# Kernel tuning notes

Hardware: AMD Instinct MI355X
Metric: run time of the kernel (lower is better)

Reference implementation:

```python
import jax, jax.numpy as jnp
import numpy as np

NUM_CENTROID = 64
HIDDEN = 768
MAX_SEQ = 128
D = MAX_SEQ * HIDDEN  # 98304 flattened feature dim
NUM_ITERS = 10        # fixed Lloyd iterations (original loops to tol; fixed for jit)


def _cdist(x, c):
    x2 = jnp.sum(x * x, axis=-1, keepdims=True)          # [N,1]
    c2 = jnp.sum(c * c, axis=-1)                          # [K]
    d2 = x2 + c2[None, :] - 2.0 * (x @ c.T)               # [N,K]
    return jnp.sqrt(jnp.maximum(d2, 0.0))


def setup_inputs() -> dict:
    key = jax.random.key(0)
    k1, k2 = jax.random.split(key)
    x = jax.random.normal(k1, (1024, MAX_SEQ, HIDDEN), dtype=jnp.float32)
    # centroid table initialized as Normal(mean=0.07, std=0.39) per the module
    centroid = 0.07 + 0.39 * jax.random.normal(k2, (NUM_CENTROID, D), dtype=jnp.float32)
    return {"x": x, "centroid": centroid}


def reference(x, centroid):
    X = x.reshape(-1, D)                                  # [N, D]
    N = X.shape[0]
    # 'resuming' branch: snap each centroid to its nearest sample
    dis0 = _cdist(X, centroid)                            # [N, K]
    choice_points = jnp.argmin(dis0, axis=0)              # [K]
    state = X[choice_points]                              # [K, D]
    ones = jnp.ones((N,), dtype=X.dtype)

    def step(state, _):
        dis = _cdist(X, state)                            # [N, K]
        choice = jnp.argmin(dis, axis=1)                  # [N]
        sums = jax.ops.segment_sum(X, choice, num_segments=NUM_CENTROID)   # [K, D]
        counts = jax.ops.segment_sum(ones, choice, num_segments=NUM_CENTROID)  # [K]
        nonempty = counts[:, None] > 0
        new_state = jnp.where(nonempty, sums / jnp.maximum(counts[:, None], 1.0), state)
        return new_state, choice

    state, choices = jax.lax.scan(step, state, None, length=NUM_ITERS)
    # returns (new centroids, final cluster assignments) like the module
    return state, choices[-1]
```

## Files before the change

kernel.cpp:

```cpp
#include <hip/hip_runtime.h>
#include <cstddef>
#include <cstdint>


#define N_PTS  1024
#define K_C    64
#define D_DIM  98304
#define ITERS  10
#define SPLITD 64
#define BM     64
#define DC     64
#define LDSP   72
#define NCHK   96
#define CCHK   12
#define NGRP   32
#define SHPG   6
#define SHW    512
#define NCHT   96
#define NPAIR  36
#define GT     128
#define GDC    32

typedef __attribute__((ext_vector_type(8))) short bf16x8;
typedef __attribute__((ext_vector_type(8))) unsigned short ushort8;
typedef __attribute__((ext_vector_type(4))) float f32x4;

__device__ __forceinline__ unsigned short f2bf(float x) {
    unsigned u = __float_as_uint(x);
    u = (u + 0x7FFFu + ((u >> 16) & 1u)) >> 16;
    return (unsigned short)u;
}
__device__ __forceinline__ float bf2f(unsigned short b) {
    return __uint_as_float((unsigned)b << 16);
}
__device__ __forceinline__ void cvt2(float x, unsigned short& h, unsigned short& l) {
    h = f2bf(x);
    l = f2bf(x - bf2f(h));
}

__device__ __forceinline__ void gload_lds16(const unsigned short* g, char* l) {
    __builtin_amdgcn_global_load_lds(
        (const __attribute__((address_space(1))) unsigned int*)g,
        (__attribute__((address_space(3))) unsigned int*)l, 16, 0, 0);
}

__device__ __forceinline__ float block_sum256(float s) {
    #pragma unroll
    for (int o = 32; o; o >>= 1) s += __shfl_down(s, o);
    __shared__ float red[4];
    int lane = threadIdx.x & 63, w = threadIdx.x >> 6;
    if (lane == 0) red[w] = s;
    __syncthreads();
    return red[0] + red[1] + red[2] + red[3];
}

__global__ __launch_bounds__(256) void convert_kernel(const float* __restrict__ A,
                                                      unsigned short* __restrict__ Ph,
                                                      unsigned short* __restrict__ Pl,
                                                      float* __restrict__ sq_part) {
    const int n = blockIdx.x, j = blockIdx.y;
    const size_t base = (size_t)n * D_DIM + (size_t)j * 8192;
    const int t = threadIdx.x;
    float ss = 0.f;
    #pragma unroll
    for (int i = 0; i < 4; ++i) {
        size_t e = base + (size_t)i * 2048 + t * 8;
        float4 a = *reinterpret_cast<const float4*>(A + e);
        float4 b = *reinterpret_cast<const float4*>(A + e + 4);
        ss += a.x*a.x + a.y*a.y + a.z*a.z + a.w*a.w;
        ss += b.x*b.x + b.y*b.y + b.z*b.z + b.w*b.w;
        ushort4 h0, l0, h1, l1;
        cvt2(a.x, h0.x, l0.x); cvt2(a.y, h0.y, l0.y);
        cvt2(a.z, h0.z, l0.z); cvt2(a.w, h0.w, l0.w);
        cvt2(b.x, h1.x, l1.x); cvt2(b.y, h1.y, l1.y);
        cvt2(b.z, h1.z, l1.z); cvt2(b.w, h1.w, l1.w);
        *reinterpret_cast<ushort4*>(Ph + e)     = h0;
        *reinterpret_cast<ushort4*>(Ph + e + 4) = h1;
        *reinterpret_cast<ushort4*>(Pl + e)     = l0;
        *reinterpret_cast<ushort4*>(Pl + e + 4) = l1;
    }
    ss = block_sum256(ss);
    if (t == 0) sq_part[n * CCHK + j] = ss;
}

__global__ __launch_bounds__(256) void reduce_sq_kernel(const float* __restrict__ sq_part,
                                                        float* __restrict__ out, int rows) {
    int n = blockIdx.x * 256 + threadIdx.x;
    if (n >= rows) return;
    float s = 0.f;
    #pragma unroll
    for (int j = 0; j < CCHK; ++j) s += sq_part[n * CCHK + j];
    out[n] = s;
}

__global__ __launch_bounds__(256) void mfma_dot_kernel(const unsigned short* __restrict__ Xh,
                                                       const unsigned short* __restrict__ Xl,
                                                       const unsigned short* __restrict__ Sh,
                                                       const unsigned short* __restrict__ Sl,
                                                       float* __restrict__ partial) {
    __shared__ alignas(16) short Bh[K_C][LDSP];
    __shared__ alignas(16) short Bl[K_C][LDSP];

    const int seg = blockIdx.x, nblk = blockIdx.y;
    const int t = threadIdx.x;
    const int wid = t >> 6, lane = t & 63;
    const int d_begin = seg * (D_DIM / SPLITD);
    const int NCH = (D_DIM / SPLITD) / DC;

    const int arow = nblk * BM + wid * 16 + (lane & 15);
    const int ko = (lane >> 4) * 8;
    const unsigned short* xh = Xh + (size_t)arow * D_DIM;
    const unsigned short* xl = Xl + (size_t)arow * D_DIM;

    const int sr = t >> 2, sc = (t & 3) * 16;
    const unsigned short* shp = Sh + (size_t)sr * D_DIM;
    const unsigned short* slp = Sl + (size_t)sr * D_DIM;

    ushort8 s0, s1, s2, s3;
    bf16x8 aEh0, aEh1, aEl0, aEl1;
    bf16x8 aOh0, aOh1, aOl0, aOl1;

    auto loadB = [&](int d0) {
        s0 = *reinterpret_cast<const ushort8*>(shp + d0 + sc);
        s1 = *reinterpret_cast<const ushort8*>(shp + d0 + sc + 8);
        s2 = *reinterpret_cast<const ushort8*>(slp + d0 + sc);
        s3 = *reinterpret_cast<const ushort8*>(slp + d0 + sc + 8);
    };
    auto storeB = [&]() {
        *reinterpret_cast<ushort8*>(&Bh[sr][sc])     = s0;
        *reinterpret_cast<ushort8*>(&Bh[sr][sc + 8]) = s1;
        *reinterpret_cast<ushort8*>(&Bl[sr][sc])     = s2;
        *reinterpret_cast<ushort8*>(&Bl[sr][sc + 8]) = s3;
    };

    f32x4 acc[4];
    #pragma unroll
    for (int i = 0; i < 4; ++i) acc[i] = f32x4{0.f, 0.f, 0.f, 0.f};

    #define LOADA(bh0, bh1, bl0, bl1, d0)                                        \
        bh0 = *reinterpret_cast<const bf16x8*>(xh + (d0) + ko);                  \
        bh1 = *reinterpret_cast<const bf16x8*>(xh + (d0) + 32 + ko);             \
        bl0 = *reinterpret_cast<const bf16x8*>(xl + (d0) + ko);                  \
        bl1 = *reinterpret_cast<const bf16x8*>(xl + (d0) + 32 + ko);

    #define MFMAS(ah0, ah1, al0, al1)                                            \
        _Pragma("unroll")                                                        \
        for (int nb = 0; nb < 4; ++nb) {                                         \
            const int br = nb * 16 + (lane & 15);                                \
            bf16x8 bh = *reinterpret_cast<const bf16x8*>(&Bh[br][ko]);           \
            bf16x8 bl = *reinterpret_cast<const bf16x8*>(&Bl[br][ko]);           \
            acc[nb] = __builtin_amdgcn_mfma_f32_16x16x32_bf16(ah0, bh, acc[nb], 0, 0, 0); \
            acc[nb] = __builtin_amdgcn_mfma_f32_16x16x32_bf16(ah0, bl, acc[nb], 0, 0, 0); \
            acc[nb] = __builtin_amdgcn_mfma_f32_16x16x32_bf16(al0, bh, acc[nb], 0, 0, 0); \
        }                                                                        \
        _Pragma("unroll")                                                        \
        for (int nb = 0; nb < 4; ++nb) {                                         \
            const int br = nb * 16 + (lane & 15);                                \
            bf16x8 bh = *reinterpret_cast<const bf16x8*>(&Bh[br][32 + ko]);      \
            bf16x8 bl = *reinterpret_cast<const bf16x8*>(&Bl[br][32 + ko]);      \
            acc[nb] = __builtin_amdgcn_mfma_f32_16x16x32_bf16(ah1, bh, acc[nb], 0, 0, 0); \
            acc[nb] = __builtin_amdgcn_mfma_f32_16x16x32_bf16(ah1, bl, acc[nb], 0, 0, 0); \
            acc[nb] = __builtin_amdgcn_mfma_f32_16x16x32_bf16(al1, bh, acc[nb], 0, 0, 0); \
        }

    loadB(d_begin);
    LOADA(aEh0, aEh1, aEl0, aEl1, d_begin);
    for (int c = 0; c < NCH; c += 2) {
        __syncthreads();
        storeB();
        __syncthreads();
        {
            int dn = d_begin + (c + 1) * DC;
            loadB(dn);
            LOADA(aOh0, aOh1, aOl0, aOl1, dn);
        }
        MFMAS(aEh0, aEh1, aEl0, aEl1);
        __syncthreads();
        storeB();
        __syncthreads();
        if (c + 2 < NCH) {
            int dn = d_begin + (c + 2) * DC;
            loadB(dn);
            LOADA(aEh0, aEh1, aEl0, aEl1, dn);
        }
        MFMAS(aOh0, aOh1, aOl0, aOl1);
    }
    #undef LOADA
    #undef MFMAS

    #pragma unroll
    for (int nb = 0; nb < 4; ++nb)
        #pragma unroll
        for (int r = 0; r < 4; ++r) {
            int row = wid * 16 + (lane >> 4) * 4 + r;
            int col = nb * 16 + (lane & 15);
            int n = nblk * BM + row;
            partial[((size_t)seg * N_PTS + n) * K_C + col] = acc[nb][r];
        }
}

__global__ __launch_bounds__(256) void reduce_dot_kernel(const float* __restrict__ partial,
                                                         float* __restrict__ dot) {
    int i = blockIdx.x * 256 + threadIdx.x;
    float s = 0.f;
    #pragma unroll 8
    for (int p = 0; p < SPLITD; ++p) s += partial[(size_t)p * N_PTS * K_C + i];
    dot[i] = s;
}

__global__ __launch_bounds__(256) void argmin_n_kernel(const float* __restrict__ dot,
                                                       const float* __restrict__ x2,
                                                       int* __restrict__ choice_pts) {
    int k = blockIdx.x;
    float best = 3.4e38f; int bi = N_PTS;
    for (int n = threadIdx.x; n < N_PTS; n += 256) {
        float v = fmaf(-2.f, dot[n * K_C + k], x2[n]);
        if (v < best || (v == best && n < bi)) { best = v; bi = n; }
    }
    #pragma unroll
    for (int off = 32; off; off >>= 1) {
        float v2 = __shfl_down(best, off);
        int   i2 = __shfl_down(bi, off);
        if (v2 < best || (v2 == best && i2 < bi)) { best = v2; bi = i2; }
    }
    __shared__ float bv[4]; __shared__ int bix[4];
    int lane = threadIdx.x & 63, wid = threadIdx.x >> 6;
    if (lane == 0) { bv[wid] = best; bix[wid] = bi; }
    __syncthreads();
    if (threadIdx.x == 0) {
        for (int w = 1; w < 4; ++w)
            if (bv[w] < best || (bv[w] == best && bix[w] < bi)) { best = bv[w]; bi = bix[w]; }
        choice_pts[k] = bi;
    }
}

__global__ __launch_bounds__(256) void gather_kernel(const float* __restrict__ X,
                                                     const int* __restrict__ choice_pts,
                                                     float* __restrict__ state) {
    int k = blockIdx.x;
    int c = choice_pts[k];
    size_t d = (size_t)blockIdx.y * 1024 + threadIdx.x * 4;
    float4 v = *reinterpret_cast<const float4*>(X + (size_t)c * D_DIM + d);
    *reinterpret_cast<float4*>(state + (size_t)k * D_DIM + d) = v;
}

__global__ __launch_bounds__(256, 3) void gbuild_kernel(const unsigned short* __restrict__ Xh,
                                                        const unsigned short* __restrict__ Xl,
                                                        float* __restrict__ Gpart) {
    __shared__ alignas(16) char LA[16384];
    __shared__ alignas(16) char LB[16384];

    const int id = blockIdx.x;
    const int xr = id & 7, q = id >> 3;
    const int p = q % NPAIR;
    const int g = ((q / NPAIR) << 3) + xr;
    int bi = 0, rem = p, rl = 8;
    while (rem >= rl) { rem -= rl; --rl; ++bi; }
    const int bj = bi + rem;

    const int t = threadIdx.x;
    const int wid = t >> 6, lane = t & 63;
    const int wr = wid >> 1, wc = wid & 1;

    const int isA = (wid < 2) ? 1 : 0;
    const int i0 = (wid & 1) * 8;
    char* ltile = isA ? LA : LB;
    const int rowbase = (isA ? bi : bj) * GT;
    const int lw = (lane & 7) ^ (lane >> 3);
    const unsigned short* plane = (lw & 4) ? Xl : Xh;
    const unsigned short* gbase[8];
    #pragma unroll
    for (int j = 0; j < 8; ++j)
        gbase[j] = plane + (size_t)(rowbase + (i0 + j) * 8 + (lane >> 3)) * D_DIM + (lw & 3) * 8;

    const int sh = (lane >> 4) ^ (lane & 7);
    const int sl = (4 + (lane >> 4)) ^ (lane & 7);
    const int ra0 = (wr * 64 + (lane & 15)) * 128;
    const int rb0 = (wc * 64 + (lane & 15)) * 128;

    f32x4 acc[4][4];
    #pragma unroll
    for (int i = 0; i < 4; ++i)
        #pragma unroll
        for (int j = 0; j < 4; ++j) acc[i][j] = f32x4{0.f, 0.f, 0.f, 0.f};

    for (int idx = 0; idx < NCHT; ++idx) {
        const int d0 = (g + ((idx >> 4) << 5)) * SHW + (idx & 15) * GDC;
        __syncthreads();
        #pragma unroll
        for (int j = 0; j < 8; ++j)
            gload_lds16(gbase[j] + d0, ltile + (i0 + j) * 1024);
        __syncthreads();
        bf16x8 ah[4], al[4];
        #pragma unroll
        for (int fi = 0; fi < 4; ++fi) {
            ah[fi] = *reinterpret_cast<const bf16x8*>(LA + ra0 + fi * 2048 + sh * 16);
            al[fi] = *reinterpret_cast<const bf16x8*>(LA + ra0 + fi * 2048 + sl * 16);
        }
        #pragma unroll
        for (int fj = 0; fj < 4; ++fj) {
            bf16x8 bh = *reinterpret_cast<const bf16x8*>(LB + rb0 + fj * 2048 + sh * 16);
            bf16x8 bl = *reinterpret_cast<const bf16x8*>(LB + rb0 + fj * 2048 + sl * 16);
            #pragma unroll
            for (int fi = 0; fi < 4; ++fi) {
                acc[fi][fj] = __builtin_amdgcn_mfma_f32_16x16x32_bf16(ah[fi], bh, acc[fi][fj], 0, 0, 0);
                acc[fi][fj] = __builtin_amdgcn_mfma_f32_16x16x32_bf16(ah[fi], bl, acc[fi][fj], 0, 0, 0);
                acc[fi][fj] = __builtin_amdgcn_mfma_f32_16x16x32_bf16(al[fi], bh, acc[fi][fj], 0, 0, 0);
            }
        }
    }

    float* gp = Gpart + ((size_t)g * NPAIR + p) * (GT * GT);
    #pragma unroll
    for (int fi = 0; fi < 4; ++fi)
        #pragma unroll
        for (int fj = 0; fj < 4; ++fj)
            #pragma unroll
            for (int r2 = 0; r2 < 4; ++r2) {
                int row = wr * 64 + fi * 16 + (lane >> 4) * 4 + r2;
                int col = wc * 64 + fj * 16 + (lane & 15);
                gp[row * GT + col] = acc[fi][fj][r2];
            }
}

__global__ __launch_bounds__(256) void reduce_g_kernel(const float* __restrict__ Gpart,
                                                       float* __restrict__ G) {
    const int p = blockIdx.x, blk = blockIdx.y;
    int bi = 0, rem = p, rl = 8;
    while (rem >= rl) { rem -= rl; --rl; ++bi; }
    const int bj = bi + rem;
    const int e0 = blk * 1024 + threadIdx.x * 4;
    float sx = 0.f, sy = 0.f, sz = 0.f, sw = 0.f;
    #pragma unroll 8
    for (int g = 0; g < NGRP; ++g) {
        const float4 v = *reinterpret_cast<const float4*>(
            Gpart + ((size_t)g * NPAIR + p) * (GT * GT) + e0);
        sx += v.x; sy += v.y; sz += v.z; sw += v.w;
    }
    const int row = e0 >> 7, col = e0 & 127;
    const int gi = bi * GT + row, gj = bj * GT + col;
    float4 o = {sx, sy, sz, sw};
    *reinterpret_cast<float4*>(&G[(size_t)gi * N_PTS + gj]) = o;
    if (bi != bj) {
        G[(size_t)(gj + 0) * N_PTS + gi] = sx;
        G[(size_t)(gj + 1) * N_PTS + gi] = sy;
        G[(size_t)(gj + 2) * N_PTS + gi] = sz;
        G[(size_t)(gj + 3) * N_PTS + gi] = sw;
    }
}

__global__ __launch_bounds__(256) void dot0_kernel(const float* __restrict__ G,
                                                   const int* __restrict__ cpts,
                                                   const float* __restrict__ x2,
                                                   float* __restrict__ dot,
                                                   float* __restrict__ c2) {
    int g = blockIdx.x * 256 + threadIdx.x;
    int n = g >> 6, k = g & 63;
    dot[g] = G[(size_t)n * N_PTS + cpts[k]];
    if (g < K_C) c2[g] = x2[cpts[g]];
}

__global__ __launch_bounds__(256) void assign_g_kernel(const float* __restrict__ dot,
                                                       const float* __restrict__ c2,
                                                       int* __restrict__ choice_it) {
    int wid = threadIdx.x >> 6, lane = threadIdx.x & 63;
    int n = blockIdx.x * 4 + wid;
    float v = fmaf(-2.f, dot[n * K_C + lane], c2[lane]);
    int bi = lane;
    #pragma unroll
    for (int m = 32; m; m >>= 1) {
        float v2 = __shfl_xor(v, m);
        int   i2 = __shfl_xor(bi, m);
        if (v2 < v || (v2 == v && i2 < bi)) { v = v2; bi = i2; }
    }
    if (lane == 0) choice_it[n] = bi;
}

__global__ __launch_bounds__(1024) void sort2_kernel(const int* __restrict__ choice,
                                                     int* __restrict__ order,
                                                     int* __restrict__ cstart,
                                                     int* __restrict__ tlast,
                                                     int it) {
    __shared__ int ch[N_PTS];
    __shared__ int cnt[K_C];
    __shared__ int cst[K_C + 1];
    int t = threadIdx.x;
    if (t < K_C) cnt[t] = 0;
    __syncthreads();
    int c = choice[t];
    ch[t] = c;
    atomicAdd(&cnt[c], 1);
    __syncthreads();
    if (t == 0) {
        int a = 0;
        for (int k = 0; k < K_C; ++k) { cst[k] = a; a += cnt[k]; }
        cst[K_C] = a;
    }
    __syncthreads();
    if (t <= K_C) cstart[t] = cst[t];
    if (t < K_C && cnt[t] > 0) tlast[t] = it;
    int r = 0;
    for (int m = 0; m < t; ++m) r += (ch[m] == c);
    order[cst[c] + r] = t;
}

__global__ __launch_bounds__(256) void dotup_kernel(const float* __restrict__ G,
                                                    const int* __restrict__ order,
                                                    const int* __restrict__ cstart,
                                                    float* __restrict__ dot) {
    __shared__ int ord[N_PTS];
    __shared__ int cst[K_C + 1];
    int t = threadIdx.x;
    #pragma unroll
    for (int i = 0; i < 4; ++i) ord[t + 256 * i] = order[t + 256 * i];
    if (t <= K_C) cst[t] = cstart[t];
    __syncthreads();
    int wid = t >> 6, lane = t & 63;
    int n = blockIdx.x * 4 + wid;
    int b = cst[lane], e = cst[lane + 1];
    if (b == e) return;
    const float* gr = G + (size_t)n * N_PTS;
    float s = 0.f;
    for (int i = b; i < e; ++i) s += gr[ord[i]];
    dot[n * K_C + lane] = s / (float)(e - b);
}

__global__ __launch_bounds__(64) void c2up_kernel(const float* __restrict__ dot,
                                                  const int* __restrict__ order,
                                                  const int* __restrict__ cstart,
                                                  float* __restrict__ c2) {
    int k = threadIdx.x;
    int b = cstart[k], e = cstart[k + 1];
    if (b == e) return;
    float s = 0.f;
    for (int i = b; i < e; ++i) s += dot[order[i] * K_C + k];
    c2[k] = s / (float)(e - b);
}

__global__ __launch_bounds__(64) void init_tlast_kernel(int* __restrict__ tlast) {
    tlast[threadIdx.x] = -1;
}

__global__ __launch_bounds__(256) void final_state_kernel(const float* __restrict__ X,
                                                          const int* __restrict__ chbuf,
                                                          const int* __restrict__ tlast,
                                                          float* __restrict__ state) {
    const int k = blockIdx.x;
    const int tk = tlast[k];
    if (tk < 0) return;
    __shared__ int chs[N_PTS];
    const int* src = chbuf + tk * N_PTS;
    const int t = threadIdx.x;
    #pragma unroll
    for (int i = 0; i < 4; ++i) chs[t + 256 * i] = src[t + 256 * i];
    __syncthreads();
    const size_t d = (size_t)blockIdx.y * 1024 + t * 4;
    float sx = 0.f, sy = 0.f, sz = 0.f, sw = 0.f;
    int cm = 0;
    for (int n = 0; n < N_PTS; ++n) {
        if (chs[n] == k) {
            ++cm;
            const float4 v = *reinterpret_cast<const float4*>(X + (size_t)n * D_DIM + d);
            sx += v.x; sy += v.y; sz += v.z; sw += v.w;
        }
    }
    float inv = 1.f / (float)cm;
    float4 o = {sx * inv, sy * inv, sz * inv, sw * inv};
    *reinterpret_cast<float4*>(state + (size_t)k * D_DIM + d) = o;
}

__global__ __launch_bounds__(256) void choice_out_kernel(const int* __restrict__ choice,
                                                         float* __restrict__ out) {
    int n = blockIdx.x * 256 + threadIdx.x;
    if (n < N_PTS) out[n] = (float)choice[n];
}

extern "C" void kernel_launch(void* const* d_in, const int* in_sizes, int n_in,
                              void* d_out, int out_size, void* d_ws, size_t ws_size,
                              hipStream_t stream) {
    const float* X  = (const float*)d_in[0];
    const float* C0 = (const float*)d_in[1];
    float* state      = (float*)d_out;
    float* out_choice = state + (size_t)K_C * D_DIM;

    char* w = (char*)d_ws;
    size_t off = 0;
    auto alloc = [&](size_t bytes) { void* p = w + off; off = (off + bytes + 255) & ~(size_t)255; return p; };
    unsigned short* Xh = (unsigned short*)alloc((size_t)N_PTS * D_DIM * 2);
    unsigned short* Xl = (unsigned short*)alloc((size_t)N_PTS * D_DIM * 2);
    unsigned short* Sh = (unsigned short*)alloc((size_t)K_C * D_DIM * 2);
    unsigned short* Sl = (unsigned short*)alloc((size_t)K_C * D_DIM * 2);
    float* partial = (float*)alloc((size_t)SPLITD * N_PTS * K_C * 4);
    float* Gpart   = (float*)alloc((size_t)NGRP * NPAIR * GT * GT * 4);
    float* G       = (float*)alloc((size_t)N_PTS * N_PTS * 4);
    float* dotb    = (float*)alloc((size_t)N_PTS * K_C * 4);
    float* x2p     = (float*)alloc((size_t)N_PTS * CCHK * 4);
    float* x2      = (float*)alloc((size_t)N_PTS * 4);
    float* c0sq    = (float*)alloc((size_t)K_C * CCHK * 4);
    float* dotg    = (float*)alloc((size_t)N_PTS * K_C * 4);
    float* c2      = (float*)alloc(256);
    int* cpts      = (int*)alloc(256);
    int* chbuf     = (int*)alloc((size_t)ITERS * N_PTS * 4);
    int* order     = (int*)alloc((size_t)N_PTS * 4);
    int* cstart    = (int*)alloc(512);
    int* tlast     = (int*)alloc(256);

    dim3 b256(256);

    convert_kernel<<<dim3(N_PTS, CCHK), b256, 0, stream>>>(X, Xh, Xl, x2p);
    reduce_sq_kernel<<<dim3(4), b256, 0, stream>>>(x2p, x2, N_PTS);

    gbuild_kernel<<<dim3(8 * NPAIR * (NGRP / 8)), b256, 0, stream>>>(Xh, Xl, Gpart);
    reduce_g_kernel<<<dim3(NPAIR, 16), b256, 0, stream>>>(Gpart, G);

    convert_kernel<<<dim3(K_C, CCHK), b256, 0, stream>>>(C0, Sh, Sl, c0sq);
    mfma_dot_kernel<<<dim3(SPLITD, N_PTS / BM), b256, 0, stream>>>(Xh, Xl, Sh, Sl, partial);
    reduce_dot_kernel<<<dim3(N_PTS * K_C / 256), b256, 0, stream>>>(partial, dotb);
    argmin_n_kernel<<<K_C, b256, 0, stream>>>(dotb, x2, cpts);
    gather_kernel<<<dim3(K_C, NCHK), b256, 0, stream>>>(X, cpts, state);
    init_tlast_kernel<<<1, dim3(64), 0, stream>>>(tlast);
    dot0_kernel<<<dim3(N_PTS * K_C / 256), b256, 0, stream>>>(G, cpts, x2, dotg, c2);

    for (int it = 0; it < ITERS; ++it) {
        assign_g_kernel<<<dim3(N_PTS / 4), b256, 0, stream>>>(dotg, c2, chbuf + it * N_PTS);
        sort2_kernel<<<1, dim3(1024), 0, stream>>>(chbuf + it * N_PTS, order, cstart, tlast, it);
        if (it < ITERS - 1) {
            dotup_kernel<<<dim3(N_PTS / 4), b256, 0, stream>>>(G, order, cstart, dotg);
            c2up_kernel<<<1, dim3(64), 0, stream>>>(dotg, order, cstart, c2);
        }
    }

    final_state_kernel<<<dim3(K_C, NCHK), b256, 0, stream>>>(X, chbuf, tlast, state);
    choice_out_kernel<<<dim3(N_PTS / 256), b256, 0, stream>>>(chbuf + (ITERS - 1) * N_PTS, out_choice);
}
```

Before: 1.928 ms.

## Fuse per-iteration assign/sort/c2 kernels and halve Gram build split groups

Merges assign_g, sort2 and c2up into a single 1024-thread step_kernel per Lloyd iteration, and folds the choice output into the last iteration, cutting the launch count in the iteration loop. Separately, the Gram-build kernel now uses 16 D-groups with twice as many chunks each, a larger LDS allocation and occupancy hint 2 instead of 3. This halves the partial Gram buffer traffic but gives fewer, longer blocks. The fused step kernel does the assignment argmin in a single workgroup, which serialises work that was spread across 256 blocks.

```diff
diff --git a/kernel.cpp b/kernel.cpp
--- a/kernel.cpp
+++ b/kernel.cpp
@@ -13,10 +13,10 @@
 #define LDSP   72
 #define NCHK   96
 #define CCHK   12
-#define NGRP   32
-#define SHPG   6
+#define NGRP   16
+#define SHPG   12
 #define SHW    512
-#define NCHT   96
+#define NCHT   192
 #define NPAIR  36
 #define GT     128
 #define GDC    32
@@ -244,11 +244,11 @@
     *reinterpret_cast<float4*>(state + (size_t)k * D_DIM + d) = v;
 }
 
-__global__ __launch_bounds__(256, 3) void gbuild_kernel(const unsigned short* __restrict__ Xh,
+__global__ __launch_bounds__(256, 2) void gbuild_kernel(const unsigned short* __restrict__ Xh,
                                                         const unsigned short* __restrict__ Xl,
                                                         float* __restrict__ Gpart) {
-    __shared__ alignas(16) char LA[16384];
-    __shared__ alignas(16) char LB[16384];
+    __shared__ alignas(16) char LA[16384 + 12288];
+    __shared__ alignas(16) char LB[16384 + 12288];
 
     const int id = blockIdx.x;
     const int xr = id & 7, q = id >> 3;
@@ -285,7 +285,7 @@
         for (int j = 0; j < 4; ++j) acc[i][j] = f32x4{0.f, 0.f, 0.f, 0.f};
 
     for (int idx = 0; idx < NCHT; ++idx) {
-        const int d0 = (g + ((idx >> 4) << 5)) * SHW + (idx & 15) * GDC;
+        const int d0 = (g + ((idx >> 4) << 4)) * SHW + (idx & 15) * GDC;
         __syncthreads();
         #pragma unroll
         for (int j = 0; j < 8; ++j)
@@ -360,35 +360,52 @@
     if (g < K_C) c2[g] = x2[cpts[g]];
 }
 
-__global__ __launch_bounds__(256) void assign_g_kernel(const float* __restrict__ dot,
-                                                       const float* __restrict__ c2,
-                                                       int* __restrict__ choice_it) {
-    int wid = threadIdx.x >> 6, lane = threadIdx.x & 63;
-    int n = blockIdx.x * 4 + wid;
-    float v = fmaf(-2.f, dot[n * K_C + lane], c2[lane]);
-    int bi = lane;
-    #pragma unroll
-    for (int m = 32; m; m >>= 1) {
-        float v2 = __shfl_xor(v, m);
-        int   i2 = __shfl_xor(bi, m);
-        if (v2 < v || (v2 == v && i2 < bi)) { v = v2; bi = i2; }
-    }
-    if (lane == 0) choice_it[n] = bi;
-}
-
-__global__ __launch_bounds__(1024) void sort2_kernel(const int* __restrict__ choice,
-                                                     int* __restrict__ order,
-                                                     int* __restrict__ cstart,
-                                                     int* __restrict__ tlast,
-                                                     int it) {
+__global__ __launch_bounds__(1024) void step_kernel(const float* __restrict__ dotg,
+                                                    float* __restrict__ c2,
+                                                    int* __restrict__ chbuf,
+                                                    int* __restrict__ order,
+                                                    int* __restrict__ cstart,
+                                                    int* __restrict__ tlast,
+                                                    int it,
+                                                    float* __restrict__ out_choice) {
     __shared__ int ch[N_PTS];
     __shared__ int cnt[K_C];
     __shared__ int cst[K_C + 1];
-    int t = threadIdx.x;
+    __shared__ float c2s[K_C];
+    const int t = threadIdx.x;
+
+    if (it > 0 && t < K_C) {
+        int b = cstart[t], e = cstart[t + 1];
+        if (b != e) {
+            float s = 0.f;
+            for (int i = b; i < e; ++i) s += dotg[order[i] * K_C + t];
+            c2[t] = s / (float)(e - b);
+        }
+    }
+    __syncthreads();
+    if (t < K_C) c2s[t] = c2[t];
+    __syncthreads();
+
+    {
+        const int wv = t >> 6, lane = t & 63;
+        const float myc2 = c2s[lane];
+        for (int n = wv * 64; n < wv * 64 + 64; ++n) {
+            float v = fmaf(-2.f, dotg[n * K_C + lane], myc2);
+            int bi = lane;
+            #pragma unroll
+            for (int m = 32; m; m >>= 1) {
+                float v2 = __shfl_xor(v, m);
+                int   i2 = __shfl_xor(bi, m);
+                if (v2 < v || (v2 == v && i2 < bi)) { v = v2; bi = i2; }
+            }
+            if (lane == 0) ch[n] = bi;
+        }
+    }
+    __syncthreads();
+
     if (t < K_C) cnt[t] = 0;
     __syncthreads();
-    int c = choice[t];
-    ch[t] = c;
+    const int c = ch[t];
     atomicAdd(&cnt[c], 1);
     __syncthreads();
     if (t == 0) {
@@ -402,6 +419,8 @@
     int r = 0;
     for (int m = 0; m < t; ++m) r += (ch[m] == c);
     order[cst[c] + r] = t;
+    chbuf[it * N_PTS + t] = c;
+    if (it == ITERS - 1) out_choice[t] = (float)c;
 }
 
 __global__ __launch_bounds__(256) void dotup_kernel(const float* __restrict__ G,
@@ -423,18 +442,6 @@
     float s = 0.f;
     for (int i = b; i < e; ++i) s += gr[ord[i]];
     dot[n * K_C + lane] = s / (float)(e - b);
-}
-
-__global__ __launch_bounds__(64) void c2up_kernel(const float* __restrict__ dot,
-                                                  const int* __restrict__ order,
-                                                  const int* __restrict__ cstart,
-                                                  float* __restrict__ c2) {
-    int k = threadIdx.x;
-    int b = cstart[k], e = cstart[k + 1];
-    if (b == e) return;
-    float s = 0.f;
-    for (int i = b; i < e; ++i) s += dot[order[i] * K_C + k];
-    c2[k] = s / (float)(e - b);
 }
 
 __global__ __launch_bounds__(64) void init_tlast_kernel(int* __restrict__ tlast) {
@@ -467,12 +474,6 @@
     float inv = 1.f / (float)cm;
     float4 o = {sx * inv, sy * inv, sz * inv, sw * inv};
     *reinterpret_cast<float4*>(state + (size_t)k * D_DIM + d) = o;
-}
-
-__global__ __launch_bounds__(256) void choice_out_kernel(const int* __restrict__ choice,
-                                                         float* __restrict__ out) {
-    int n = blockIdx.x * 256 + threadIdx.x;
-    if (n < N_PTS) out[n] = (float)choice[n];
 }
 
 extern "C" void kernel_launch(void* const* d_in, const int* in_sizes, int n_in,
@@ -522,14 +523,11 @@
     dot0_kernel<<<dim3(N_PTS * K_C / 256), b256, 0, stream>>>(G, cpts, x2, dotg, c2);
 
     for (int it = 0; it < ITERS; ++it) {
-        assign_g_kernel<<<dim3(N_PTS / 4), b256, 0, stream>>>(dotg, c2, chbuf + it * N_PTS);
-        sort2_kernel<<<1, dim3(1024), 0, stream>>>(chbuf + it * N_PTS, order, cstart, tlast, it);
-        if (it < ITERS - 1) {
+        step_kernel<<<1, dim3(1024), 0, stream>>>(dotg, c2, chbuf, order, cstart,
+                                                  tlast, it, out_choice);
+        if (it < ITERS - 1)
             dotup_kernel<<<dim3(N_PTS / 4), b256, 0, stream>>>(G, order, cstart, dotg);
-            c2up_kernel<<<1, dim3(64), 0, stream>>>(dotg, order, cstart, c2);
-        }
     }
 
     final_state_kernel<<<dim3(K_C, NCHK), b256, 0, stream>>>(X, chbuf, tlast, state);
-    choice_out_kernel<<<dim3(N_PTS / 256), b256, 0, stream>>>(chbuf + (ITERS - 1) * N_PTS, out_choice);
-}
+}
```

Result: slower. 2.436 ms (+26.4%).
